# Optimization experiments

Measured on AMD Instinct MI355X. Metric: run time of the kernel, lower is better.

## Reference

```python
import jax, jax.numpy as jnp
import numpy as np

B, E, S, H = 8, 1024, 2048, 16  # batch, embed_dim, seq_len, n_heads
D = E // H                       # per-head hidden dim


def setup_inputs() -> dict:
    key = jax.random.key(0)
    k1, k2 = jax.random.split(key)
    x = jax.random.normal(k1, (B, E, S), dtype=jnp.float32)
    weight = jax.random.normal(k2, (H, S), dtype=jnp.float32)  # nn.Parameter(torch.randn)
    bias = jnp.zeros((H, S), dtype=jnp.float32)                # nn.Parameter(torch.zeros)
    return {"x": x, "weight": weight, "bias": bias}


def _vector_to_matrix(v):
    # v: (H, S) -> M: (H, S, S), M[h, i, j] = v[h, j - i] if j >= i else 0
    h, m = v.shape
    i = jnp.arange(m)[:, None]
    j = jnp.arange(m)[None, :]
    off = j - i  # negative offsets wrap (same as torch fancy indexing) but are masked out
    return jnp.where(j >= i, v[:, off], jnp.zeros((), dtype=v.dtype))


def reference(x, weight, bias):
    b, e, s = x.shape
    h = weight.shape[0]
    d = e // h
    M = _vector_to_matrix(weight)  # (H, S, S)
    # Original: x.view(B,H,D,S).reshape(B*H,D,S) paired with W.repeat_interleave(B,0),
    # i.e. flat index k uses M[k // B]. Group the flat B*H axis into H contiguous
    # blocks of size B so each block shares one Toeplitz matrix (no (B*H,S,S) blowup).
    xg = x.reshape(b * h, d, s).reshape(h, b, d, s)  # block m = M[m]
    out = jnp.einsum('mbds,mst->mbdt', xg, M) + bias[:, None, None, :]
    return out.reshape(b, e, s)
```

## Files before the change

kernel.cpp:

```cpp
#include <hip/hip_runtime.h>
#include <hip/hip_bf16.h>

#define SEQ    2048
#define NHEAD  16
#define RPH    512
#define BM     128
#define BK     64
#define NTH    256

#define WSTRIDE 2184
#define ABUF_E  8192
#define WCOP_E  (2 * ABUF_E)
#define TOT_E   (WCOP_E + 8 * WSTRIDE)

typedef float  f32x4  __attribute__((ext_vector_type(4)));
typedef __bf16 bf16x8 __attribute__((ext_vector_type(8)));

struct PF { float4 v0, v1, v2, v3, v4, v5, v6, v7; };

__device__ __forceinline__ unsigned f2bf(float f) {
    union { __hip_bfloat16 h; unsigned short u; } cv;
    cv.h = __float2bfloat16(f);
    return (unsigned)cv.u;
}

__device__ __forceinline__ uint4 pack8u(float4 a, float4 b) {
    union { bf16x8 v; uint4 u; } r;
    r.v[0] = (__bf16)a.x; r.v[1] = (__bf16)a.y;
    r.v[2] = (__bf16)a.z; r.v[3] = (__bf16)a.w;
    r.v[4] = (__bf16)b.x; r.v[5] = (__bf16)b.y;
    r.v[6] = (__bf16)b.z; r.v[7] = (__bf16)b.w;
    return r.u;
}

#define MFMA16(a, b, c) __builtin_amdgcn_mfma_f32_16x16x32_bf16((a), (b), (c), 0, 0, 0)

#define LOADPF(P, CH)                                                         \
  { const float* g_ = Xp + (size_t)(CH) * BK;                                 \
    P.v0 = *(const float4*)g_;                                                \
    P.v1 = *(const float4*)(g_ + 4);                                          \
    P.v2 = *(const float4*)(g_ + 8 * SEQ);                                    \
    P.v3 = *(const float4*)(g_ + 8 * SEQ + 4);                                \
    P.v4 = *(const float4*)(g_ + 16 * SEQ);                                   \
    P.v5 = *(const float4*)(g_ + 16 * SEQ + 4);                               \
    P.v6 = *(const float4*)(g_ + 24 * SEQ);                                   \
    P.v7 = *(const float4*)(g_ + 24 * SEQ + 4); }

#define WRITEA(AB, P)                                                         \
  { *(uint4*)((AB) + wb0) = pack8u(P.v0, P.v1);                               \
    *(uint4*)((AB) + wb1) = pack8u(P.v2, P.v3);                               \
    *(uint4*)((AB) + wb2) = pack8u(P.v4, P.v5);                               \
    *(uint4*)((AB) + wb3) = pack8u(P.v6, P.v7); }

#define WINLOAD4(CH, OFFE, S0, S1, S2, S3)                                    \
  { const unsigned short* bq_ = wcB + 64 * (CH) + (OFFE);                     \
    bw[S0] = *(const bf16x8*)(bq_);                                           \
    bw[S1] = *(const bf16x8*)(bq_ + 16);                                      \
    bw[S2] = *(const bf16x8*)(bq_ + 32);                                      \
    bw[S3] = *(const bf16x8*)(bq_ + 48); }

#define KSTEPW(ABC, KS, P8, BASE)                                             \
  { const int kb_ = (64 * (KS) + kq16) ^ swz;                                 \
    bf16x8 af0 = *(const bf16x8*)((ABC) + Arow0 + kb_);                       \
    bf16x8 af1 = *(const bf16x8*)((ABC) + Arow1 + kb_);                       \
    acc[0][0] = MFMA16(af0, bw[((P8)+(BASE)-0)&15], acc[0][0]);               \
    acc[1][0] = MFMA16(af1, bw[((P8)+(BASE)-0)&15], acc[1][0]);               \
    acc[0][1] = MFMA16(af0, bw[((P8)+(BASE)-1)&15], acc[0][1]);               \
    acc[1][1] = MFMA16(af1, bw[((P8)+(BASE)-1)&15], acc[1][1]);               \
    acc[0][2] = MFMA16(af0, bw[((P8)+(BASE)-2)&15], acc[0][2]);               \
    acc[1][2] = MFMA16(af1, bw[((P8)+(BASE)-2)&15], acc[1][2]);               \
    acc[0][3] = MFMA16(af0, bw[((P8)+(BASE)-3)&15], acc[0][3]);               \
    acc[1][3] = MFMA16(af1, bw[((P8)+(BASE)-3)&15], acc[1][3]);               \
    acc[0][4] = MFMA16(af0, bw[((P8)+(BASE)-4)&15], acc[0][4]);               \
    acc[1][4] = MFMA16(af1, bw[((P8)+(BASE)-4)&15], acc[1][4]);               \
    acc[0][5] = MFMA16(af0, bw[((P8)+(BASE)-5)&15], acc[0][5]);               \
    acc[1][5] = MFMA16(af1, bw[((P8)+(BASE)-5)&15], acc[1][5]);               \
    acc[0][6] = MFMA16(af0, bw[((P8)+(BASE)-6)&15], acc[0][6]);               \
    acc[1][6] = MFMA16(af1, bw[((P8)+(BASE)-6)&15], acc[1][6]);               \
    acc[0][7] = MFMA16(af0, bw[((P8)+(BASE)-7)&15], acc[0][7]);               \
    acc[1][7] = MFMA16(af1, bw[((P8)+(BASE)-7)&15], acc[1][7]); }

#define PAIRBODY(P8)                                                          \
  {                                                                           \
    WRITEA(ab1, pfB);                                                         \
    if (ch + 3 < nch) LOADPF(pfB, ch + 3);                                    \
    __builtin_amdgcn_s_setprio(1);                                            \
    KSTEPW(ab0, 0, P8, 7);                                                    \
    KSTEPW(ab0, 1, P8, 9);                                                    \
    __builtin_amdgcn_s_setprio(0);                                            \
    if (ch + 2 < nch)                                                         \
        WINLOAD4(ch, 112, ((P8)+14)&15, ((P8)+15)&15,                         \
                 ((P8)+16)&15, ((P8)+17)&15);                                 \
    if (ch + 2 < nch) WRITEA(ab0, pfA);                                       \
    if (ch + 4 < nch) LOADPF(pfA, ch + 4);                                    \
    __builtin_amdgcn_s_setprio(1);                                            \
    KSTEPW(ab1, 0, P8, 11);                                                   \
    KSTEPW(ab1, 1, P8, 13);                                                   \
    __builtin_amdgcn_s_setprio(0);                                            \
    if (ch + 2 < nch)                                                         \
        WINLOAD4(ch, 176, ((P8)+18)&15, ((P8)+19)&15,                         \
                 ((P8)+20)&15, ((P8)+21)&15);                                 \
  }

__global__ __launch_bounds__(NTH, 2) void mixer_kernel(
    const float* __restrict__ x, const float* __restrict__ wgt,
    const float* __restrict__ bias, float* __restrict__ out)
{
    __shared__ unsigned short smem[TOT_E] __attribute__((aligned(16)));
    char* ab0 = (char*)smem;
    char* ab1 = (char*)smem + ABUF_E * 2;
    unsigned short* wc = smem + WCOP_E;

    const int tid  = threadIdx.x;
    const int lane = tid & 63;
    const int wv   = tid >> 6;

    const int bid  = blockIdx.x;
    const int m    = (bid & 7) + 8 * ((bid >> 3) & 1);
    const int rt   = (bid >> 4) & 3;
    const int pr   = bid >> 6;
    const int ct_hi = 15 - pr;
    const int ct_lo = pr;

    const float* Xb = x   + (size_t)(m * RPH + rt * BM) * SEQ;
    float*       Ob = out + (size_t)(m * RPH + rt * BM) * SEQ;
    const float* wr = wgt  + m * SEQ;
    const float* br = bias + m * SEQ;

    const int sr    = lane >> 3;
    const int sc    = (lane & 7) * 8;
    const int wsw   = ((lane & 7) * 16) ^ (sr << 4);
    const int rbw   = 32 * wv;
    const int wb0   = (rbw + sr)      * 128 + wsw;
    const int wb1   = (rbw + sr + 8)  * 128 + wsw;
    const int wb2   = (rbw + sr + 16) * 128 + wsw;
    const int wb3   = (rbw + sr + 24) * 128 + wsw;
    const float* Xp = Xb + (size_t)(rbw + sr) * SEQ + sc;

    PF pfA, pfB;
    LOADPF(pfA, 0);
    LOADPF(pfB, 1);

    {
        const int t8 = tid * 8;
        const float* g = wr + (2040 - t8);
        float4 lo = *(const float4*)g;
        float4 hi = *(const float4*)(g + 4);
        uint4 v;
        v.x = f2bf(hi.w) | (f2bf(hi.z) << 16);
        v.y = f2bf(hi.y) | (f2bf(hi.x) << 16);
        v.z = f2bf(lo.w) | (f2bf(lo.z) << 16);
        v.w = f2bf(lo.y) | (f2bf(lo.x) << 16);
        *(uint4*)(smem + 8 + t8) = v;
        if (tid < 21) {
            uint4 z = {0u, 0u, 0u, 0u};
            unsigned short* dst = (tid == 0) ? smem
                                 : smem + 8 + 2048 + (tid - 1) * 8;
            *(uint4*)dst = z;
        }
    }
    __syncthreads();

    #pragma unroll
    for (int c = 0; c < 8; ++c) {
        for (int grp = tid; grp < WSTRIDE / 8; grp += NTH) {
            const int i = grp * 8;
            uint4 g0 = *(const uint4*)(smem + 8 + i - 8);
            uint4 g1 = *(const uint4*)(smem + 8 + i);
            unsigned d[9] = {g0.x, g0.y, g0.z, g0.w,
                             g1.x, g1.y, g1.z, g1.w, 0u};
            const int qd = (16 - 2 * c) >> 2;
            uint4 o;
            if (c & 1) {
                o.x = (d[qd]     >> 16) | (d[qd + 1] << 16);
                o.y = (d[qd + 1] >> 16) | (d[qd + 2] << 16);
                o.z = (d[qd + 2] >> 16) | (d[qd + 3] << 16);
                o.w = (d[qd + 3] >> 16) | (d[qd + 4] << 16);
            } else {
                o.x = d[qd];     o.y = d[qd + 1];
                o.z = d[qd + 2]; o.w = d[qd + 3];
            }
            *(uint4*)(wc + c * WSTRIDE + i) = o;
        }
    }
    __syncthreads();

    const int col_low = lane & 15;
    const int kq      = lane >> 4;
    const int kq16    = kq * 16;
    const int swz     = (col_low & 7) << 4;
    const int cpy     = (col_low + 1) & 7;
    const int BcBase  = cpy * WSTRIDE + cpy + 2047 - col_low + 8 * kq;
    const int Arow0   = (rbw      + col_low) * 128;
    const int Arow1   = (rbw + 16 + col_low) * 128;

    #pragma unroll
    for (int half = 0; half < 2; ++half) {
        const int ct  = half ? ct_lo : ct_hi;
        const int t0  = ct << 7;
        const int nch = 2 * (ct + 1);
        const unsigned short* wcB = wc + (BcBase - t0);

        if (half) { LOADPF(pfA, 0); LOADPF(pfB, 1); }

        WRITEA(ab0, pfA);
        if (2 < nch) LOADPF(pfA, 2);

        bf16x8 bw[16];
        {
            const unsigned short* bq_ = wcB - 112;
            #pragma unroll
            for (int i = 0; i < 14; ++i)
                bw[i] = *(const bf16x8*)(bq_ + 16 * i);
        }

        f32x4 acc[2][8] = {};
        int ch = 0;
        for (;;) {
            PAIRBODY(0);
            ch += 2; if (ch >= nch) break;
            PAIRBODY(8);
            ch += 2; if (ch >= nch) break;
        }

        #pragma unroll
        for (int c = 0; c < 8; ++c) {
            const int colg = t0 + 16 * c + col_low;
            const float bv = br[colg];
            #pragma unroll
            for (int a = 0; a < 2; ++a) {
                const int rowl = rbw + 16 * a + 4 * kq;
                #pragma unroll
                for (int r = 0; r < 4; ++r)
                    Ob[(size_t)(rowl + r) * SEQ + colg] = acc[a][c][r] + bv;
            }
        }
    }
}

extern "C" void kernel_launch(void* const* d_in, const int* in_sizes, int n_in,
                              void* d_out, int out_size, void* d_ws, size_t ws_size,
                              hipStream_t stream) {
    const float* x  = (const float*)d_in[0];
    const float* w  = (const float*)d_in[1];
    const float* bs = (const float*)d_in[2];
    float* out = (float*)d_out;
    dim3 grid(512);
    dim3 block(NTH);
    hipLaunchKernelGGL(mixer_kernel, grid, block, 0, stream, x, w, bs, out);
}
```

Baseline: 47.01 us.

## Use 512-thread blocks with two wave groups sharing A tiles across adjacent column tiles

Each block now runs 8 waves. Two groups of four waves compute adjacent 128-column output tiles (256j and 256j+128) over a shared cooperatively loaded A (x) stream. Before, one block of 4 waves processed two complementary column tiles in sequence. The A-tile staging is split across twice as many threads with explicit barriers, and per-group chunk limits skip the MFMA steps that the causal Toeplitz structure makes zero. This is meant to halve redundant x loads across column tiles and balance the triangular work. In exchange it adds per-chunk barriers and drops occupancy to one block per CU, and blocks now carry uneven work (j from 0 to 7).

```diff
diff --git a/kernel.cpp b/kernel.cpp
--- a/kernel.cpp
+++ b/kernel.cpp
@@ -6,17 +6,17 @@
 #define RPH    512
 #define BM     128
 #define BK     64
-#define NTH    256
+#define NTH    512
 
 #define WSTRIDE 2184
 #define ABUF_E  8192
 #define WCOP_E  (2 * ABUF_E)
-#define TOT_E   (WCOP_E + 8 * WSTRIDE)
+#define TOT_E   (WCOP_E + 8 * WSTRIDE + 128)
 
 typedef float  f32x4  __attribute__((ext_vector_type(4)));
 typedef __bf16 bf16x8 __attribute__((ext_vector_type(8)));
 
-struct PF { float4 v0, v1, v2, v3, v4, v5, v6, v7; };
+struct PF { float4 v0, v1, v2, v3; };
 
 __device__ __forceinline__ unsigned f2bf(float f) {
     union { __hip_bfloat16 h; unsigned short u; } cv;
@@ -39,18 +39,12 @@
   { const float* g_ = Xp + (size_t)(CH) * BK;                                 \
     P.v0 = *(const float4*)g_;                                                \
     P.v1 = *(const float4*)(g_ + 4);                                          \
-    P.v2 = *(const float4*)(g_ + 8 * SEQ);                                    \
-    P.v3 = *(const float4*)(g_ + 8 * SEQ + 4);                                \
-    P.v4 = *(const float4*)(g_ + 16 * SEQ);                                   \
-    P.v5 = *(const float4*)(g_ + 16 * SEQ + 4);                               \
-    P.v6 = *(const float4*)(g_ + 24 * SEQ);                                   \
-    P.v7 = *(const float4*)(g_ + 24 * SEQ + 4); }
+    P.v2 = *(const float4*)(g_ + 8);                                          \
+    P.v3 = *(const float4*)(g_ + 12); }
 
 #define WRITEA(AB, P)                                                         \
   { *(uint4*)((AB) + wb0) = pack8u(P.v0, P.v1);                               \
-    *(uint4*)((AB) + wb1) = pack8u(P.v2, P.v3);                               \
-    *(uint4*)((AB) + wb2) = pack8u(P.v4, P.v5);                               \
-    *(uint4*)((AB) + wb3) = pack8u(P.v6, P.v7); }
+    *(uint4*)((AB) + wb1) = pack8u(P.v2, P.v3); }
 
 #define WINLOAD4(CH, OFFE, S0, S1, S2, S3)                                    \
   { const unsigned short* bq_ = wcB + 64 * (CH) + (OFFE);                     \
@@ -82,27 +76,33 @@
 
 #define PAIRBODY(P8)                                                          \
   {                                                                           \
-    WRITEA(ab1, pfB);                                                         \
+    WRITEA(ab1, pfB);                         \
     if (ch + 3 < nch) LOADPF(pfB, ch + 3);                                    \
-    __builtin_amdgcn_s_setprio(1);                                            \
-    KSTEPW(ab0, 0, P8, 7);                                                    \
-    KSTEPW(ab0, 1, P8, 9);                                                    \
-    __builtin_amdgcn_s_setprio(0);                                            \
+    if (ch < nchw) {                                                          \
+      __builtin_amdgcn_s_setprio(1);                                          \
+      KSTEPW(ab0, 0, P8, 7);                                                  \
+      KSTEPW(ab0, 1, P8, 9);                                                  \
+      __builtin_amdgcn_s_setprio(0);                                          \
+    }                                                                         \
     if (ch + 2 < nch)                                                         \
         WINLOAD4(ch, 112, ((P8)+14)&15, ((P8)+15)&15,                         \
                  ((P8)+16)&15, ((P8)+17)&15);                                 \
-    if (ch + 2 < nch) WRITEA(ab0, pfA);                                       \
+    asm volatile("s_waitcnt lgkmcnt(0)\n\ts_barrier" ::: "memory");           \
+    if (ch + 2 < nch) WRITEA(ab0, pfA);       \
     if (ch + 4 < nch) LOADPF(pfA, ch + 4);                                    \
-    __builtin_amdgcn_s_setprio(1);                                            \
-    KSTEPW(ab1, 0, P8, 11);                                                   \
-    KSTEPW(ab1, 1, P8, 13);                                                   \
-    __builtin_amdgcn_s_setprio(0);                                            \
+    if (ch + 1 < nchw) {                                                      \
+      __builtin_amdgcn_s_setprio(1);                                          \
+      KSTEPW(ab1, 0, P8, 11);                                                 \
+      KSTEPW(ab1, 1, P8, 13);                                                 \
+      __builtin_amdgcn_s_setprio(0);                                          \
+    }                                                                         \
     if (ch + 2 < nch)                                                         \
         WINLOAD4(ch, 176, ((P8)+18)&15, ((P8)+19)&15,                         \
                  ((P8)+20)&15, ((P8)+21)&15);                                 \
+    asm volatile("s_waitcnt lgkmcnt(0)\n\ts_barrier" ::: "memory");           \
   }
 
-__global__ __launch_bounds__(NTH, 2) void mixer_kernel(
+__global__ __launch_bounds__(NTH, 1) void mixer_kernel(
     const float* __restrict__ x, const float* __restrict__ wgt,
     const float* __restrict__ bias, float* __restrict__ out)
 {
@@ -114,34 +114,33 @@
     const int tid  = threadIdx.x;
     const int lane = tid & 63;
     const int wv   = tid >> 6;
+    const int r    = wv & 3;
+    const int tb   = wv >> 2;
 
     const int bid  = blockIdx.x;
     const int m    = (bid & 7) + 8 * ((bid >> 3) & 1);
     const int rt   = (bid >> 4) & 3;
-    const int pr   = bid >> 6;
-    const int ct_hi = 15 - pr;
-    const int ct_lo = pr;
+    const int j    = 7 - (bid >> 6);
+    const int nch  = 4 * j + 4;
+    const int nchw = nch - 2 + 2 * tb;
 
     const float* Xb = x   + (size_t)(m * RPH + rt * BM) * SEQ;
     float*       Ob = out + (size_t)(m * RPH + rt * BM) * SEQ;
     const float* wr = wgt  + m * SEQ;
     const float* br = bias + m * SEQ;
 
-    const int sr    = lane >> 3;
-    const int sc    = (lane & 7) * 8;
-    const int wsw   = ((lane & 7) * 16) ^ (sr << 4);
-    const int rbw   = 32 * wv;
-    const int wb0   = (rbw + sr)      * 128 + wsw;
-    const int wb1   = (rbw + sr + 8)  * 128 + wsw;
-    const int wb2   = (rbw + sr + 16) * 128 + wsw;
-    const int wb3   = (rbw + sr + 24) * 128 + wsw;
-    const float* Xp = Xb + (size_t)(rbw + sr) * SEQ + sc;
+    const int srow = 32 * r + 16 * tb + (lane >> 2);
+    const int colq = lane & 3;
+    const int wsw  = (srow & 7) << 4;
+    const int wb0  = srow * 128 + ((colq * 32) ^ wsw);
+    const int wb1  = srow * 128 + ((colq * 32 + 16) ^ wsw);
+    const float* Xp = Xb + (size_t)srow * SEQ + colq * 16;
 
     PF pfA, pfB;
     LOADPF(pfA, 0);
     LOADPF(pfB, 1);
 
-    {
+    if (tid < 256) {
         const int t8 = tid * 8;
         const float* g = wr + (2040 - t8);
         float4 lo = *(const float4*)g;
@@ -189,51 +188,45 @@
     const int kq      = lane >> 4;
     const int kq16    = kq * 16;
     const int swz     = (col_low & 7) << 4;
+    const int rbw     = 32 * r;
+    const int t0w     = 256 * j + 128 * tb;
     const int cpy     = (col_low + 1) & 7;
     const int BcBase  = cpy * WSTRIDE + cpy + 2047 - col_low + 8 * kq;
     const int Arow0   = (rbw      + col_low) * 128;
     const int Arow1   = (rbw + 16 + col_low) * 128;
+    const unsigned short* wcB = wc + (BcBase - t0w);
+
+    WRITEA(ab0, pfA);
+    LOADPF(pfA, 2);
+
+    bf16x8 bw[16];
+    {
+        const unsigned short* bq_ = wcB - 112;
+        #pragma unroll
+        for (int i = 0; i < 14; ++i)
+            bw[i] = *(const bf16x8*)(bq_ + 16 * i);
+    }
+    __syncthreads();
+
+    f32x4 acc[2][8] = {};
+    int ch = 0;
+    for (;;) {
+        PAIRBODY(0);
+        ch += 2; if (ch >= nch) break;
+        PAIRBODY(8);
+        ch += 2; if (ch >= nch) break;
+    }
 
     #pragma unroll
-    for (int half = 0; half < 2; ++half) {
-        const int ct  = half ? ct_lo : ct_hi;
-        const int t0  = ct << 7;
-        const int nch = 2 * (ct + 1);
-        const unsigned short* wcB = wc + (BcBase - t0);
-
-        if (half) { LOADPF(pfA, 0); LOADPF(pfB, 1); }
-
-        WRITEA(ab0, pfA);
-        if (2 < nch) LOADPF(pfA, 2);
-
-        bf16x8 bw[16];
-        {
-            const unsigned short* bq_ = wcB - 112;
+    for (int c = 0; c < 8; ++c) {
+        const int colg = t0w + 16 * c + col_low;
+        const float bv = br[colg];
+        #pragma unroll
+        for (int a = 0; a < 2; ++a) {
+            const int rowl = rbw + 16 * a + 4 * kq;
             #pragma unroll
-            for (int i = 0; i < 14; ++i)
-                bw[i] = *(const bf16x8*)(bq_ + 16 * i);
-        }
-
-        f32x4 acc[2][8] = {};
-        int ch = 0;
-        for (;;) {
-            PAIRBODY(0);
-            ch += 2; if (ch >= nch) break;
-            PAIRBODY(8);
-            ch += 2; if (ch >= nch) break;
-        }
-
-        #pragma unroll
-        for (int c = 0; c < 8; ++c) {
-            const int colg = t0 + 16 * c + col_low;
-            const float bv = br[colg];
-            #pragma unroll
-            for (int a = 0; a < 2; ++a) {
-                const int rowl = rbw + 16 * a + 4 * kq;
-                #pragma unroll
-                for (int r = 0; r < 4; ++r)
-                    Ob[(size_t)(rowl + r) * SEQ + colg] = acc[a][c][r] + bv;
-            }
+            for (int rr = 0; rr < 4; ++rr)
+                Ob[(size_t)(rowl + rr) * SEQ + colg] = acc[a][c][rr] + bv;
         }
     }
 }
```

Result: faster. 44.70 us (-4.9%).
